# Kernel tuning notes

Measured on AMD Instinct MI355X. Metric: run time of the kernel, lower is better.

The kernel has to match this reference:

```python
import jax, jax.numpy as jnp
import numpy as np

N_PTS = 1048576
N_FEATS = 32
GRID = (96, 96, 96)
L = 6                      # num_positional_encoding_terms
D_IN = N_FEATS + 2 * L * 3  # 68
H_DIM = 128
VMIN, VMAX = -1.0, 1.0


def setup_inputs() -> dict:
    key = jax.random.key(0)
    ks = jax.random.split(key, 5)
    def lin(k, shp, fan):
        return jax.random.normal(k, shp, jnp.float32) * (1.0 / np.sqrt(fan).astype(np.float32))
    return {
        "x": jax.random.uniform(ks[0], (N_PTS, 3), jnp.float32),          # coords in [0,1) subset of [-1,1]
        "feature_grid": jax.random.uniform(ks[1], (1, N_FEATS) + GRID, jnp.float32),
        "W0": lin(ks[2], (H_DIM, D_IN), D_IN), "b0": jnp.zeros((H_DIM,), jnp.float32),
        "W1": lin(ks[3], (H_DIM, H_DIM), H_DIM), "b1": jnp.zeros((H_DIM,), jnp.float32),
        "W2": lin(ks[4], (1, H_DIM), H_DIM), "b2": jnp.zeros((1,), jnp.float32),
    }


def positional_encoding(x):
    # x: [N, d] -> [N, 2*L*d], NeRF-style: per frequency 2^i * pi, [sin | cos]
    freqs = jnp.pi * (2.0 ** jnp.arange(L, dtype=jnp.float32))   # [L]
    xf = x[:, None, :] * freqs[None, :, None]                    # [N, L, d]
    return jnp.concatenate([jnp.sin(xf), jnp.cos(xf)], axis=-1).reshape(x.shape[0], -1)


def grid_sample_3d(grid, coords):
    # Trilinear F.grid_sample, align_corners=True.
    # grid: [C, D, H, W]; coords: [N, 3] in [-1,1], ordered (x, y, z) -> (W, H, D)
    C, D, H, W = grid.shape
    def unnorm(c, size):
        return (c + 1.0) * 0.5 * (size - 1)
    fx, fy, fz = unnorm(coords[:, 0], W), unnorm(coords[:, 1], H), unnorm(coords[:, 2], D)
    x0, y0, z0 = jnp.floor(fx), jnp.floor(fy), jnp.floor(fz)
    wx, wy, wz = fx - x0, fy - y0, fz - z0
    def ci(i, size):
        return jnp.clip(i.astype(jnp.int32), 0, size - 1)
    x0i, x1i = ci(x0, W), ci(x0 + 1, W)
    y0i, y1i = ci(y0, H), ci(y0 + 1, H)
    z0i, z1i = ci(z0, D), ci(z0 + 1, D)
    def g(zi, yi, xi):
        return grid[:, zi, yi, xi]   # irregular gather -> [C, N]
    return (g(z0i, y0i, x0i) * ((1 - wz) * (1 - wy) * (1 - wx))
          + g(z0i, y0i, x1i) * ((1 - wz) * (1 - wy) * wx)
          + g(z0i, y1i, x0i) * ((1 - wz) * wy * (1 - wx))
          + g(z0i, y1i, x1i) * ((1 - wz) * wy * wx)
          + g(z1i, y0i, x0i) * (wz * (1 - wy) * (1 - wx))
          + g(z1i, y0i, x1i) * (wz * (1 - wy) * wx)
          + g(z1i, y1i, x0i) * (wz * wy * (1 - wx))
          + g(z1i, y1i, x1i) * (wz * wy * wx))   # [C, N]


def reference(x, feature_grid, W0, b0, W1, b1, W2, b2):
    feats = grid_sample_3d(feature_grid[0], x).T                       # [N, C]
    h = jnp.concatenate([positional_encoding(x), feats], axis=1)       # [N, 68]
    h = jax.nn.relu(h @ W0.T + b0)                                     # [N, 128]
    h = jax.nn.relu(h @ W1.T + b1)                                     # [N, 128]
    y = h @ W2.T + b2                                                  # [N, 1]
    return y * (VMAX - VMIN) + VMIN
```

## Files before the change

### kernel.cpp

```cpp
#include <hip/hip_runtime.h>

#define NPTS 1048576
#define NCH 32
#define GS 96
#define GV (GS * GS * GS)
#define DIN 68
#define HD 128
#define TILE_PTS 32
#define NTILES (NPTS / TILE_PTS)
#define NBLK 256
#define NTHR 768
#define WAVES_TOT (NBLK * 12)

typedef __bf16 bf16x8 __attribute__((ext_vector_type(8)));
typedef float f32x4 __attribute__((ext_vector_type(4)));
typedef float f32x2 __attribute__((ext_vector_type(2)));

__device__ __forceinline__ unsigned int f2bf(float f) {
  unsigned int u = __float_as_uint(f);
  return (u + 0x7fffu + ((u >> 16) & 1u)) >> 16;
}
__device__ __forceinline__ unsigned int pkbf(float a, float b) {
  return f2bf(a) | (f2bf(b) << 16);
}
__device__ __forceinline__ unsigned int cvtpk(float a, float b) {
  unsigned int r;
  asm("v_cvt_pk_bf16_f32 %0, %1, %2" : "=v"(r) : "v"(a), "v"(b));
  return r;
}

__global__ __launch_bounds__(256) void k_prep_grid(const float* __restrict__ src,
                                                   unsigned int* __restrict__ dst) {
  __shared__ unsigned int tile[256 * 17];
  const int tid = threadIdx.x;
  const long vb = (long)blockIdx.x * 256;
  const int c2 = tid >> 4;
  const int vgb = tid & 15;
#pragma unroll
  for (int p = 0; p < 4; ++p) {
    int vox = (vgb + p * 16) * 4;
    const float4 a = *(const float4*)(src + (long)(2 * c2) * GV + vb + vox);
    const float4 b = *(const float4*)(src + (long)(2 * c2 + 1) * GV + vb + vox);
    tile[(vox + 0) * 17 + c2] = pkbf(a.x, b.x);
    tile[(vox + 1) * 17 + c2] = pkbf(a.y, b.y);
    tile[(vox + 2) * 17 + c2] = pkbf(a.z, b.z);
    tile[(vox + 3) * 17 + c2] = pkbf(a.w, b.w);
  }
  __syncthreads();
  const int vox2 = tid >> 2;
  const int c4 = (tid & 3) * 4;
#pragma unroll
  for (int j = 0; j < 4; ++j) {
    int vx = vox2 + j * 64;
    uint4 w;
    w.x = tile[vx * 17 + c4 + 0];
    w.y = tile[vx * 17 + c4 + 1];
    w.z = tile[vx * 17 + c4 + 2];
    w.w = tile[vx * 17 + c4 + 3];
    *(uint4*)(dst + (vb + vx) * 16 + c4) = w;
  }
}

template <bool TA>
__global__ __launch_bounds__(NTHR, 3) void k_fvsrn(
    const float* __restrict__ X, const float* __restrict__ gridF,
    const unsigned short* __restrict__ gridT,
    const float* __restrict__ W0, const float* __restrict__ B0,
    const float* __restrict__ W1, const float* __restrict__ B1,
    const float* __restrict__ W2, const float* __restrict__ B2,
    float* __restrict__ out) {
  extern __shared__ char smem[];
  float* lb0 = (float*)(smem + 57344);
  float* lb1 = (float*)(smem + 57856);
  float* lw2 = (float*)(smem + 58368);
  const int tid = threadIdx.x;

  for (int idx = tid; idx < 56 * 64; idx += NTHR) {
    int f = idx >> 6;
    int L = idx & 63;
    int qq = L >> 4, lnn = L & 15;
    float vals[8];
    if (f < 24) {
      int kt = f >> 3, nt = f & 7;
      int n = nt * 16 + lnn;
      int kb = kt * 32 + qq * 8;
#pragma unroll
      for (int j = 0; j < 8; ++j) {
        int k = kb + j;
        float w = 0.f;
        if (k < 32) w = W0[n * DIN + 36 + k];
        else if (k < DIN) w = W0[n * DIN + (k - 32)];
        vals[j] = w;
      }
    } else {
      int g = f - 24;
      int kt = g >> 3, nt = g & 7;
      int n = nt * 16 + lnn;
      int kb = kt * 32 + qq * 8;
#pragma unroll
      for (int j = 0; j < 8; ++j) vals[j] = W1[n * HD + kb + j];
    }
    uint4 pk;
    pk.x = pkbf(vals[0], vals[1]);
    pk.y = pkbf(vals[2], vals[3]);
    pk.z = pkbf(vals[4], vals[5]);
    pk.w = pkbf(vals[6], vals[7]);
    *(uint4*)(smem + f * 1024 + L * 16) = pk;
  }
  if (tid < 128) lb0[tid] = B0[tid];
  else if (tid < 256) lb1[tid - 128] = B1[tid - 128];
  else if (tid < 384) lw2[tid - 256] = W2[tid - 256];
  __syncthreads();

  const int wave = tid >> 6, lane = tid & 63;
  char* scr = smem + 58880 + wave * 8192;
  const int q = lane >> 4, ln = lane & 15;
  const int half = lane >> 5, pt = lane & 31;
  const int mtg = pt >> 4, pmg = pt & 15;
  const float b2s = B2[0];

  int t = blockIdx.x * 12 + wave;
  float px = 0.f, py = 0.f, pz = 0.f;
  if (t < NTILES) {
    long p = (long)t * TILE_PTS + pt;
    px = X[p * 3 + 0]; py = X[p * 3 + 1]; pz = X[p * 3 + 2];
  }

  for (; t < NTILES;) {
    const int tn = t + WAVES_TOT;
    const long p0 = (long)t * TILE_PTS;

    uint4 ga[8], gb[8];
    float w8[8];
    {
      float fx = (px + 1.f) * 0.5f * (GS - 1);
      float fy = (py + 1.f) * 0.5f * (GS - 1);
      float fz = (pz + 1.f) * 0.5f * (GS - 1);
      float flx = floorf(fx), fly = floorf(fy), flz = floorf(fz);
      float wx = fx - flx, wy = fy - fly, wz = fz - flz;
      int jx = (int)flx, jy = (int)fly, jz = (int)flz;
      int x0 = min(max(jx, 0), GS - 1), x1 = min(max(jx + 1, 0), GS - 1);
      int y0 = min(max(jy, 0), GS - 1) * GS, y1 = min(max(jy + 1, 0), GS - 1) * GS;
      int z0 = min(max(jz, 0), GS - 1) * (GS * GS), z1 = min(max(jz + 1, 0), GS - 1) * (GS * GS);
      if constexpr (TA) {
#pragma unroll
        for (int c = 0; c < 8; ++c) {
          int vi = (c & 4 ? z1 : z0) + (c & 2 ? y1 : y0) + (c & 1 ? x1 : x0);
          const uint4* gp = (const uint4*)(gridT + vi * NCH + 16 * half);
          ga[c] = gp[0];
          gb[c] = gp[1];
        }
      }
      float ux0 = 1.f - wx, uy0 = 1.f - wy, uz0 = 1.f - wz;
#pragma unroll
      for (int c = 0; c < 8; ++c)
        w8[c] = (c & 4 ? wz : uz0) * (c & 2 ? wy : uy0) * (c & 1 ? wx : ux0);
      if constexpr (!TA) {
#pragma unroll
        for (int c = 0; c < 8; ++c) {
          int vi = (c & 4 ? z1 : z0) + (c & 2 ? y1 : y0) + (c & 1 ? x1 : x0);
#pragma unroll
          for (int i = 0; i < 8; ++i) {
            int ch = 16 * half + 2 * i;
            unsigned int lo = f2bf(gridF[(long)ch * GV + vi]);
            unsigned int hi = f2bf(gridF[(long)(ch + 1) * GV + vi]);
            if (i < 4) { ((unsigned int*)&ga[c])[i] = lo | (hi << 16); }
            else       { ((unsigned int*)&gb[c])[i - 4] = lo | (hi << 16); }
          }
        }
      }
    }

    float v36[36];
    {
      float cc[3] = {px, py, pz};
#pragma unroll
      for (int ax = 0; ax < 3; ++ax) {
        float hrev = 0.5f * cc[ax];
        float s, co;
        asm("v_sin_f32 %0, %1" : "=v"(s) : "v"(hrev));
        asm("v_cos_f32 %0, %1" : "=v"(co) : "v"(hrev));
#pragma unroll
        for (int i = 0; i < 6; ++i) {
          v36[i * 6 + ax] = s;
          v36[i * 6 + 3 + ax] = co;
          float s2 = 2.f * s * co;
          co = 1.f - 2.f * s * s;
          s = s2;
        }
      }
    }
    unsigned int pd[8], e0, e1;
    if (half == 0) {
#pragma unroll
      for (int d = 0; d < 8; ++d) pd[d] = cvtpk(v36[2 * d], v36[2 * d + 1]);
      e0 = cvtpk(v36[32], v36[33]);
      e1 = cvtpk(v36[34], v36[35]);
    } else {
#pragma unroll
      for (int d = 0; d < 8; ++d) pd[d] = cvtpk(v36[16 + 2 * d], v36[17 + 2 * d]);
      e0 = 0u; e1 = 0u;
    }

    f32x2 f2[8];
#pragma unroll
    for (int i = 0; i < 8; ++i) f2[i] = (f32x2){0.f, 0.f};
#pragma unroll
    for (int c = 0; c < 8; ++c) {
      f32x2 w2 = {w8[c], w8[c]};
#define ACC_PAIR(u, i)                                                     \
  {                                                                        \
    f32x2 u2 = {__uint_as_float((u) << 16),                                \
                __uint_as_float((u) & 0xffff0000u)};                       \
    f2[i] = __builtin_elementwise_fma(u2, w2, f2[i]);                      \
  }
      ACC_PAIR(ga[c].x, 0) ACC_PAIR(ga[c].y, 1) ACC_PAIR(ga[c].z, 2) ACC_PAIR(ga[c].w, 3)
      ACC_PAIR(gb[c].x, 4) ACC_PAIR(gb[c].y, 5) ACC_PAIR(gb[c].z, 6) ACC_PAIR(gb[c].w, 7)
#undef ACC_PAIR
    }

    {
      char* fbase = scr + (mtg * 3) * 1024;
      int ro = pmg * 16;
      uint4 s;
      s.x = cvtpk(f2[0].x, f2[0].y); s.y = cvtpk(f2[1].x, f2[1].y);
      s.z = cvtpk(f2[2].x, f2[2].y); s.w = cvtpk(f2[3].x, f2[3].y);
      *(uint4*)(fbase + (2 * half) * 256 + ro) = s;
      s.x = cvtpk(f2[4].x, f2[4].y); s.y = cvtpk(f2[5].x, f2[5].y);
      s.z = cvtpk(f2[6].x, f2[6].y); s.w = cvtpk(f2[7].x, f2[7].y);
      *(uint4*)(fbase + (2 * half + 1) * 256 + ro) = s;
      s.x = pd[0]; s.y = pd[1]; s.z = pd[2]; s.w = pd[3];
      *(uint4*)(fbase + 1024 + (2 * half) * 256 + ro) = s;
      s.x = pd[4]; s.y = pd[5]; s.z = pd[6]; s.w = pd[7];
      *(uint4*)(fbase + 1024 + (2 * half + 1) * 256 + ro) = s;
      s.x = e0; s.y = e1; s.z = 0u; s.w = 0u;
      *(uint4*)(fbase + 2048 + (2 * half) * 256 + ro) = s;
      s.x = 0u; s.y = 0u; s.z = 0u; s.w = 0u;
      *(uint4*)(fbase + 2048 + (2 * half + 1) * 256 + ro) = s;
    }
    __builtin_amdgcn_wave_barrier();

    if (tn < NTILES) {
      long p = (long)tn * TILE_PTS + pt;
      px = X[p * 3 + 0]; py = X[p * 3 + 1]; pz = X[p * 3 + 2];
    }

    bf16x8 a0[6];
#pragma unroll
    for (int mt = 0; mt < 2; ++mt)
#pragma unroll
      for (int kt = 0; kt < 3; ++kt)
        a0[mt * 3 + kt] = *(const bf16x8*)(scr + (mt * 3 + kt) * 1024 + lane * 16);
    __builtin_amdgcn_wave_barrier();
#pragma unroll
    for (int nt = 0; nt < 8; ++nt) {
      float bn = lb0[nt * 16 + ln];
      f32x4 cinit = {bn, bn, bn, bn};
      f32x4 acc[2];
      acc[0] = cinit; acc[1] = cinit;
#pragma unroll
      for (int kt = 0; kt < 3; ++kt) {
        bf16x8 bfr = *(const bf16x8*)(smem + (kt * 8 + nt) * 1024 + lane * 16);
#pragma unroll
        for (int mt = 0; mt < 2; ++mt)
          acc[mt] = __builtin_amdgcn_mfma_f32_16x16x32_bf16(a0[mt * 3 + kt], bfr, acc[mt], 0, 0, 0);
      }
      int n = nt * 16 + ln;
      int kt1 = n >> 5, j = n & 7, sub = (n >> 3) & 3;
#pragma unroll
      for (int mt = 0; mt < 2; ++mt) {
        f32x4 zz = {0.f, 0.f, 0.f, 0.f};
        f32x4 h = __builtin_elementwise_max(acc[mt], zz);
        char* base = scr + (mt * 4 + kt1) * 1024 + (sub * 16 + q * 4) * 16 + j * 2;
        unsigned int u01 = cvtpk(h[0], h[1]);
        unsigned int u23 = cvtpk(h[2], h[3]);
        *(unsigned short*)(base + 0)  = (unsigned short)u01;
        *(unsigned short*)(base + 16) = (unsigned short)(u01 >> 16);
        *(unsigned short*)(base + 32) = (unsigned short)u23;
        *(unsigned short*)(base + 48) = (unsigned short)(u23 >> 16);
      }
    }
    __builtin_amdgcn_wave_barrier();

    bf16x8 a1[8];
#pragma unroll
    for (int mt = 0; mt < 2; ++mt)
#pragma unroll
      for (int kt = 0; kt < 4; ++kt)
        a1[mt * 4 + kt] = *(const bf16x8*)(scr + (mt * 4 + kt) * 1024 + lane * 16);
    __builtin_amdgcn_wave_barrier();
    float y[8];
#pragma unroll
    for (int i = 0; i < 8; ++i) y[i] = 0.f;
#pragma unroll
    for (int nt = 0; nt < 8; ++nt) {
      float bn = lb1[nt * 16 + ln];
      float w2n = lw2[nt * 16 + ln];
      f32x4 cinit = {bn, bn, bn, bn};
      f32x4 acc[2];
      acc[0] = cinit; acc[1] = cinit;
#pragma unroll
      for (int kt = 0; kt < 4; ++kt) {
        bf16x8 bfr = *(const bf16x8*)(smem + 24576 + (kt * 8 + nt) * 1024 + lane * 16);
#pragma unroll
        for (int mt = 0; mt < 2; ++mt)
          acc[mt] = __builtin_amdgcn_mfma_f32_16x16x32_bf16(a1[mt * 4 + kt], bfr, acc[mt], 0, 0, 0);
      }
#pragma unroll
      for (int mt = 0; mt < 2; ++mt)
#pragma unroll
        for (int r = 0; r < 4; ++r)
          y[mt * 4 + r] += w2n * fmaxf(acc[mt][r], 0.f);
    }
#pragma unroll
    for (int i = 0; i < 8; ++i) {
      float v = y[i];
      v += __shfl_xor(v, 1);
      v += __shfl_xor(v, 2);
      v += __shfl_xor(v, 4);
      v += __shfl_xor(v, 8);
      y[i] = v;
    }
    if (ln == 0) {
#pragma unroll
      for (int mt = 0; mt < 2; ++mt)
#pragma unroll
        for (int r = 0; r < 4; ++r)
          out[p0 + mt * 16 + q * 4 + r] = (y[mt * 4 + r] + b2s) * 2.f - 1.f;
    }
    t = tn;
  }
}

extern "C" void kernel_launch(void* const* d_in, const int* in_sizes, int n_in,
                              void* d_out, int out_size, void* d_ws, size_t ws_size,
                              hipStream_t stream) {
  const float* X  = (const float*)d_in[0];
  const float* G  = (const float*)d_in[1];
  const float* W0 = (const float*)d_in[2];
  const float* B0 = (const float*)d_in[3];
  const float* W1 = (const float*)d_in[4];
  const float* B1 = (const float*)d_in[5];
  const float* W2 = (const float*)d_in[6];
  const float* B2 = (const float*)d_in[7];
  float* out = (float*)d_out;

  const size_t needT = (size_t)GV * NCH * 2;
  const size_t shmem = 157184;

  if (ws_size >= needT) {
    k_prep_grid<<<GV / 256, 256, 0, stream>>>(G, (unsigned int*)d_ws);
    k_fvsrn<true><<<NBLK, NTHR, shmem, stream>>>(
        X, G, (const unsigned short*)d_ws, W0, B0, W1, B1, W2, B2, out);
  } else {
    k_fvsrn<false><<<NBLK, NTHR, shmem, stream>>>(
        X, G, (const unsigned short*)nullptr, W0, B0, W1, B1, W2, B2, out);
  }
}
```

Baseline: 289.0 us.

## Software-pipeline grid gathers for next tile across layer-1 MFMA work

Moves the eight-corner grid gather for the next tile so it is issued before the second MLP layer of the current tile, with a prologue gather before the loop. Sched barriers pin the issue points so the gather latency overlaps MFMA compute instead of stalling at the start of each iteration. The cost is 64 extra live VGPRs for the in-flight gather registers, which may pressure occupancy under the 768-thread launch bound.

```diff
diff --git a/kernel.cpp b/kernel.cpp
--- a/kernel.cpp
+++ b/kernel.cpp
@@ -58,6 +58,25 @@
     w.z = tile[vx * 17 + c4 + 2];
     w.w = tile[vx * 17 + c4 + 3];
     *(uint4*)(dst + (vb + vx) * 16 + c4) = w;
+  }
+}
+
+__device__ __forceinline__ void issue_gather(const unsigned short* __restrict__ gridT,
+                                             int half, float px, float py, float pz,
+                                             uint4 (&ga)[8], uint4 (&gb)[8]) {
+  float fx = (px + 1.f) * 0.5f * (GS - 1);
+  float fy = (py + 1.f) * 0.5f * (GS - 1);
+  float fz = (pz + 1.f) * 0.5f * (GS - 1);
+  int jx = (int)floorf(fx), jy = (int)floorf(fy), jz = (int)floorf(fz);
+  int x0 = min(max(jx, 0), GS - 1), x1 = min(max(jx + 1, 0), GS - 1);
+  int y0 = min(max(jy, 0), GS - 1) * GS, y1 = min(max(jy + 1, 0), GS - 1) * GS;
+  int z0 = min(max(jz, 0), GS - 1) * (GS * GS), z1 = min(max(jz + 1, 0), GS - 1) * (GS * GS);
+#pragma unroll
+  for (int c = 0; c < 8; ++c) {
+    int vi = (c & 4 ? z1 : z0) + (c & 2 ? y1 : y0) + (c & 1 ? x1 : x0);
+    const uint4* gp = (const uint4*)(gridT + vi * NCH + 16 * half);
+    ga[c] = gp[0];
+    gb[c] = gp[1];
   }
 }
 
@@ -126,50 +145,15 @@
     px = X[p * 3 + 0]; py = X[p * 3 + 1]; pz = X[p * 3 + 2];
   }
 
+  uint4 ga[8], gb[8];
+  if constexpr (TA) {
+    if (t < NTILES) issue_gather(gridT, half, px, py, pz, ga, gb);
+    __builtin_amdgcn_sched_barrier(0);
+  }
+
   for (; t < NTILES;) {
     const int tn = t + WAVES_TOT;
     const long p0 = (long)t * TILE_PTS;
-
-    uint4 ga[8], gb[8];
-    float w8[8];
-    {
-      float fx = (px + 1.f) * 0.5f * (GS - 1);
-      float fy = (py + 1.f) * 0.5f * (GS - 1);
-      float fz = (pz + 1.f) * 0.5f * (GS - 1);
-      float flx = floorf(fx), fly = floorf(fy), flz = floorf(fz);
-      float wx = fx - flx, wy = fy - fly, wz = fz - flz;
-      int jx = (int)flx, jy = (int)fly, jz = (int)flz;
-      int x0 = min(max(jx, 0), GS - 1), x1 = min(max(jx + 1, 0), GS - 1);
-      int y0 = min(max(jy, 0), GS - 1) * GS, y1 = min(max(jy + 1, 0), GS - 1) * GS;
-      int z0 = min(max(jz, 0), GS - 1) * (GS * GS), z1 = min(max(jz + 1, 0), GS - 1) * (GS * GS);
-      if constexpr (TA) {
-#pragma unroll
-        for (int c = 0; c < 8; ++c) {
-          int vi = (c & 4 ? z1 : z0) + (c & 2 ? y1 : y0) + (c & 1 ? x1 : x0);
-          const uint4* gp = (const uint4*)(gridT + vi * NCH + 16 * half);
-          ga[c] = gp[0];
-          gb[c] = gp[1];
-        }
-      }
-      float ux0 = 1.f - wx, uy0 = 1.f - wy, uz0 = 1.f - wz;
-#pragma unroll
-      for (int c = 0; c < 8; ++c)
-        w8[c] = (c & 4 ? wz : uz0) * (c & 2 ? wy : uy0) * (c & 1 ? wx : ux0);
-      if constexpr (!TA) {
-#pragma unroll
-        for (int c = 0; c < 8; ++c) {
-          int vi = (c & 4 ? z1 : z0) + (c & 2 ? y1 : y0) + (c & 1 ? x1 : x0);
-#pragma unroll
-          for (int i = 0; i < 8; ++i) {
-            int ch = 16 * half + 2 * i;
-            unsigned int lo = f2bf(gridF[(long)ch * GV + vi]);
-            unsigned int hi = f2bf(gridF[(long)(ch + 1) * GV + vi]);
-            if (i < 4) { ((unsigned int*)&ga[c])[i] = lo | (hi << 16); }
-            else       { ((unsigned int*)&gb[c])[i - 4] = lo | (hi << 16); }
-          }
-        }
-      }
-    }
 
     float v36[36];
     {
@@ -200,6 +184,40 @@
 #pragma unroll
       for (int d = 0; d < 8; ++d) pd[d] = cvtpk(v36[16 + 2 * d], v36[17 + 2 * d]);
       e0 = 0u; e1 = 0u;
+    }
+
+    float w8[8];
+    {
+      float fx = (px + 1.f) * 0.5f * (GS - 1);
+      float fy = (py + 1.f) * 0.5f * (GS - 1);
+      float fz = (pz + 1.f) * 0.5f * (GS - 1);
+      float wx = fx - floorf(fx), wy = fy - floorf(fy), wz = fz - floorf(fz);
+      float ux = 1.f - wx, uy = 1.f - wy, uz = 1.f - wz;
+#pragma unroll
+      for (int c = 0; c < 8; ++c)
+        w8[c] = (c & 4 ? wz : uz) * (c & 2 ? wy : uy) * (c & 1 ? wx : ux);
+    }
+
+    if constexpr (!TA) {
+      float fx = (px + 1.f) * 0.5f * (GS - 1);
+      float fy = (py + 1.f) * 0.5f * (GS - 1);
+      float fz = (pz + 1.f) * 0.5f * (GS - 1);
+      int jx = (int)floorf(fx), jy = (int)floorf(fy), jz = (int)floorf(fz);
+      int x0 = min(max(jx, 0), GS - 1), x1 = min(max(jx + 1, 0), GS - 1);
+      int y0 = min(max(jy, 0), GS - 1) * GS, y1 = min(max(jy + 1, 0), GS - 1) * GS;
+      int z0 = min(max(jz, 0), GS - 1) * (GS * GS), z1 = min(max(jz + 1, 0), GS - 1) * (GS * GS);
+#pragma unroll
+      for (int c = 0; c < 8; ++c) {
+        int vi = (c & 4 ? z1 : z0) + (c & 2 ? y1 : y0) + (c & 1 ? x1 : x0);
+#pragma unroll
+        for (int i = 0; i < 8; ++i) {
+          int ch = 16 * half + 2 * i;
+          unsigned int lo = f2bf(gridF[(long)ch * GV + vi]);
+          unsigned int hi = f2bf(gridF[(long)(ch + 1) * GV + vi]);
+          if (i < 4) { ((unsigned int*)&ga[c])[i] = lo | (hi << 16); }
+          else       { ((unsigned int*)&gb[c])[i - 4] = lo | (hi << 16); }
+        }
+      }
     }
 
     f32x2 f2[8];
@@ -240,10 +258,12 @@
     }
     __builtin_amdgcn_wave_barrier();
 
+    float px2 = 0.f, py2 = 0.f, pz2 = 0.f;
     if (tn < NTILES) {
       long p = (long)tn * TILE_PTS + pt;
-      px = X[p * 3 + 0]; py = X[p * 3 + 1]; pz = X[p * 3 + 2];
-    }
+      px2 = X[p * 3 + 0]; py2 = X[p * 3 + 1]; pz2 = X[p * 3 + 2];
+    }
+    __builtin_amdgcn_sched_barrier(0);
 
     bf16x8 a0[6];
 #pragma unroll
@@ -289,6 +309,12 @@
       for (int kt = 0; kt < 4; ++kt)
         a1[mt * 4 + kt] = *(const bf16x8*)(scr + (mt * 4 + kt) * 1024 + lane * 16);
     __builtin_amdgcn_wave_barrier();
+
+    if constexpr (TA) {
+      if (tn < NTILES) issue_gather(gridT, half, px2, py2, pz2, ga, gb);
+      __builtin_amdgcn_sched_barrier(0);
+    }
+
     float y[8];
 #pragma unroll
     for (int i = 0; i < 8; ++i) y[i] = 0.f;
@@ -328,6 +354,7 @@
         for (int r = 0; r < 4; ++r)
           out[p0 + mt * 16 + q * 4 + r] = (y[mt * 4 + r] + b2s) * 2.f - 1.f;
     }
+    px = px2; py = py2; pz = pz2;
     t = tn;
   }
 }
```

Measured after the change: 305.2 us. 1.06x slower.
